# Optimization experiments

Hardware: AMD Instinct MI355X
Metric: run time of the kernel (lower is better)

Reference implementation:

```python
import jax, jax.numpy as jnp
import numpy as np

BITW = 1
BITA = 3
BATCH = 8192
IN_CH = 4096
N_UNITS = 4096


def _quantize(x, k):
    # DoReFa uniform quantizer with straight-through estimator (round -> identity grad)
    n = float(2 ** k - 1)
    return x + jax.lax.stop_gradient(jnp.round(x * n) / n - x)


def _cabs(x):
    # clip magnitude to [0, 1]
    return jnp.minimum(1.0, jnp.abs(x))


def quantize_active(x, bitA):
    if bitA == 32:
        return x
    return _quantize(x, bitA)


def quantize_weight(w, bitW):
    if bitW == 32:
        return w
    if bitW == 1:
        # binary weights scaled by mean |w| (E is treated as constant)
        E = jax.lax.stop_gradient(jnp.mean(jnp.abs(w)))
        y = w / E
        # sign with straight-through gradient
        return (y + jax.lax.stop_gradient(jnp.sign(y) - y)) * E
    t = jnp.tanh(w)
    t = t / jnp.max(jnp.abs(t)) * 0.5 + 0.5
    return 2.0 * _quantize(t, bitW) - 1.0


def setup_inputs() -> dict:
    key = jax.random.key(0)
    k1, k2 = jax.random.split(key)
    inputs = jax.random.normal(k1, (BATCH, IN_CH), dtype=jnp.float32)
    # truncated_normal(stddev=0.1) init approximated with normal * 0.1
    W = jax.random.normal(k2, (IN_CH, N_UNITS), dtype=jnp.float32) * 0.1
    b = jnp.zeros((N_UNITS,), dtype=jnp.float32)
    return {"inputs": inputs, "W": W, "b": b}


def reference(inputs, W, b):
    q_in = quantize_active(_cabs(inputs), BITA)   # [B, IN] in {0..1} grid of 2^bitA-1 levels
    q_W = quantize_weight(W, BITW)                # [IN, OUT] binary (+-E)
    out = jnp.matmul(q_in, q_W) + b               # [B, OUT]
    return out
```

## Files before the change

kernel.cpp:

```cpp
#include <hip/hip_runtime.h>


static constexpr int BATCH  = 8192;
static constexpr int IN_CH  = 4096;
static constexpr int NUNITS = 4096;
static constexpr int TPB    = 256;

typedef int v4i __attribute__((ext_vector_type(4)));

static constexpr size_t A8_OFF   = 0;
static constexpr size_t A8_BYTES = (size_t)BATCH * IN_CH;
static constexpr size_t BT_OFF   = A8_OFF + A8_BYTES;
static constexpr size_t BT_BYTES = (size_t)NUNITS * IN_CH;
static constexpr int    NPART    = 4096;
static constexpr size_t PART_OFF = BT_OFF + BT_BYTES;
static constexpr size_t SCALE_OFF= PART_OFF + NPART * sizeof(float);

__global__ __launch_bounds__(TPB) void k_scale(const float* __restrict__ partials,
                                               float* __restrict__ scale) {
    __shared__ float red[TPB];
    float s = 0.f;
    for (int i = threadIdx.x; i < NPART; i += TPB) s += partials[i];
    red[threadIdx.x] = s;
    __syncthreads();
    for (int off = TPB / 2; off > 0; off >>= 1) {
        if ((int)threadIdx.x < off) red[threadIdx.x] += red[threadIdx.x + off];
        __syncthreads();
    }
    if (threadIdx.x == 0) {
        float E = red[0] / (float)((size_t)IN_CH * NUNITS);
        *scale = E / 7.0f;
    }
}

__device__ __forceinline__ unsigned int q4(float4 v) {
    unsigned int b0 = (unsigned int)(int)rintf(fminf(1.0f, fabsf(v.x)) * 7.0f);
    unsigned int b1 = (unsigned int)(int)rintf(fminf(1.0f, fabsf(v.y)) * 7.0f);
    unsigned int b2 = (unsigned int)(int)rintf(fminf(1.0f, fabsf(v.z)) * 7.0f);
    unsigned int b3 = (unsigned int)(int)rintf(fminf(1.0f, fabsf(v.w)) * 7.0f);
    return b0 | (b1 << 8) | (b2 << 16) | (b3 << 24);
}

__global__ __launch_bounds__(TPB) void k_quant_a(const float4* __restrict__ x4,
                                                 uint4* __restrict__ a16) {
    const size_t t = (size_t)blockIdx.x * TPB + threadIdx.x;
    uint4 o;
    o.x = q4(x4[t * 4 + 0]);
    o.y = q4(x4[t * 4 + 1]);
    o.z = q4(x4[t * 4 + 2]);
    o.w = q4(x4[t * 4 + 3]);
    a16[t] = o;
}

__global__ __launch_bounds__(TPB) void k_signT(const float* __restrict__ W,
                                               char* __restrict__ bt,
                                               float* __restrict__ partials) {
    __shared__ char tile[64][68];
    __shared__ float red[TPB];
    const int bk = blockIdx.x & 63;
    const int bn = blockIdx.x >> 6;
    const int t  = threadIdx.x;
    const int c  = t & 63;
    const int r0 = t >> 6;
    float asum = 0.f;
#pragma unroll
    for (int i = 0; i < 16; ++i) {
        int r = i * 4 + r0;
        float w = W[(size_t)(bk * 64 + r) * NUNITS + bn * 64 + c];
        asum += fabsf(w);
        tile[c][r] = (w > 0.f) ? 1 : ((w < 0.f) ? -1 : 0);
    }
    __syncthreads();
    const int n  = t >> 2;
    const int kk = (t & 3) * 16;
    char o[16];
#pragma unroll
    for (int j = 0; j < 16; ++j) o[j] = tile[n][kk + j];
    *(uint4*)(bt + (size_t)(bn * 64 + n) * IN_CH + bk * 64 + kk) = *(const uint4*)o;

    red[t] = asum;
    __syncthreads();
    for (int off = TPB / 2; off > 0; off >>= 1) {
        if (t < off) red[t] += red[t + off];
        __syncthreads();
    }
    if (t == 0) partials[blockIdx.x] = red[0];
}

__device__ __forceinline__ void gload_lds16(const void* g, void* l) {
    __builtin_amdgcn_global_load_lds((const __attribute__((address_space(1))) void*)g,
                                     (__attribute__((address_space(3))) void*)l,
                                     16, 0, 0);
}

#define VMCNT8   asm volatile("s_waitcnt vmcnt(8)" ::: "memory")
#define VMCNT0   asm volatile("s_waitcnt vmcnt(0)" ::: "memory")
#define LGKM0    asm volatile("s_waitcnt lgkmcnt(0)" ::: "memory")
#define SCHEDB   __builtin_amdgcn_sched_barrier(0)
#define BARRIER  __builtin_amdgcn_s_barrier()

static constexpr int NT = IN_CH / 128;

__global__ __launch_bounds__(512, 2) void k_gemm(const char* __restrict__ A8,
                                                 const char* __restrict__ BT,
                                                 const float* __restrict__ scale_p,
                                                 const float* __restrict__ bias,
                                                 float* __restrict__ out) {
    __shared__ char As[2][32768];
    __shared__ char Bs[2][32768];

    const int t    = threadIdx.x;
    const int bid  = blockIdx.x;
    const int swzb = (bid & 7) * 64 + (bid >> 3);
    const int bRow = swzb >> 4;
    const int bCol = swzb & 15;
    const int lane = t & 63;
    const int wid  = t >> 6;
    const int wm   = wid >> 2;
    const int wn   = wid & 3;
    const int lr   = lane & 15;
    const int lk4  = lane >> 4;

    const size_t aBase = (size_t)(bRow * 256) * IN_CH;
    const size_t bBase = (size_t)(bCol * 256) * IN_CH;

    const int ceff0 = (lk4 * 16) ^ ((lr & 7) << 4);
    const int ceff1 = ceff0 ^ 64;

    const int srow  = t >> 3;
    const int scol  = ((t & 7) * 16) ^ ((srow & 7) << 4);
    const int sldso = t * 16;

    v4i acc[8][4] = {};

#define STAGE(kt, q)                                                                 \
    do {                                                                             \
        const int _b = (kt) & 1;                                                     \
        if ((q) < 4)                                                                 \
            gload_lds16(A8 + aBase + (size_t)((q) * 64 + srow) * IN_CH + (kt) * 128 + scol, \
                        &As[_b][(q & 3) * 8192 + sldso]);                            \
        else                                                                         \
            gload_lds16(BT + bBase + (size_t)(((q) - 4) * 64 + srow) * IN_CH + (kt) * 128 + scol, \
                        &Bs[_b][((q) - 4) * 8192 + sldso]);                          \
    } while (0)

#pragma unroll
    for (int q = 0; q < 8; ++q) STAGE(0, q);
#pragma unroll
    for (int q = 0; q < 8; ++q) STAGE(1, q);

    for (int kt = 0; kt < NT; ++kt) {
        const int buf = kt & 1;
        const char* Ab = As[buf];
        const char* Bb = Bs[buf];

        if (kt < NT - 1) { VMCNT8; } else { VMCNT0; }
        SCHEDB;
        BARRIER;
        v4i a0[4][2], a1[4][2], bf[4][2];
#pragma unroll
        for (int m = 0; m < 4; ++m) {
            const int ra0 = (wm * 128 + m * 16 + lr) * 128;
            const int ra1 = (wm * 128 + (m + 4) * 16 + lr) * 128;
            a0[m][0] = *(const v4i*)(Ab + ra0 + ceff0);
            a0[m][1] = *(const v4i*)(Ab + ra0 + ceff1);
            a1[m][0] = *(const v4i*)(Ab + ra1 + ceff0);
            a1[m][1] = *(const v4i*)(Ab + ra1 + ceff1);
        }
#pragma unroll
        for (int n = 0; n < 4; ++n) {
            const int rb = (wn * 64 + n * 16 + lr) * 128;
            bf[n][0] = *(const v4i*)(Bb + rb + ceff0);
            bf[n][1] = *(const v4i*)(Bb + rb + ceff1);
        }
        LGKM0;
        SCHEDB;
        BARRIER;
        __builtin_amdgcn_s_setprio(1);
#pragma unroll
        for (int m = 0; m < 4; ++m)
#pragma unroll
            for (int n = 0; n < 2; ++n)
#pragma unroll
                for (int s = 0; s < 2; ++s)
                    acc[m][n] = __builtin_amdgcn_mfma_i32_16x16x64_i8(a0[m][s], bf[n][s], acc[m][n], 0, 0, 0);
        __builtin_amdgcn_s_setprio(0);
        SCHEDB;

        if (kt + 2 < NT) { STAGE(kt + 2, 0); STAGE(kt + 2, 1); STAGE(kt + 2, 2); }
        SCHEDB;
        BARRIER;
        __builtin_amdgcn_s_setprio(1);
#pragma unroll
        for (int m = 0; m < 4; ++m)
#pragma unroll
            for (int n = 2; n < 4; ++n)
#pragma unroll
                for (int s = 0; s < 2; ++s)
                    acc[m][n] = __builtin_amdgcn_mfma_i32_16x16x64_i8(a0[m][s], bf[n][s], acc[m][n], 0, 0, 0);
        __builtin_amdgcn_s_setprio(0);
        SCHEDB;

        if (kt + 2 < NT) { STAGE(kt + 2, 3); STAGE(kt + 2, 4); STAGE(kt + 2, 5); }
        SCHEDB;
        BARRIER;
        __builtin_amdgcn_s_setprio(1);
#pragma unroll
        for (int m = 0; m < 4; ++m)
#pragma unroll
            for (int n = 0; n < 2; ++n)
#pragma unroll
                for (int s = 0; s < 2; ++s)
                    acc[m + 4][n] = __builtin_amdgcn_mfma_i32_16x16x64_i8(a1[m][s], bf[n][s], acc[m + 4][n], 0, 0, 0);
        __builtin_amdgcn_s_setprio(0);
        SCHEDB;

        if (kt + 2 < NT) { STAGE(kt + 2, 6); STAGE(kt + 2, 7); }
        SCHEDB;
        BARRIER;
        __builtin_amdgcn_s_setprio(1);
#pragma unroll
        for (int m = 0; m < 4; ++m)
#pragma unroll
            for (int n = 2; n < 4; ++n)
#pragma unroll
                for (int s = 0; s < 2; ++s)
                    acc[m + 4][n] = __builtin_amdgcn_mfma_i32_16x16x64_i8(a1[m][s], bf[n][s], acc[m + 4][n], 0, 0, 0);
        __builtin_amdgcn_s_setprio(0);
        SCHEDB;
    }

    const float scale = *scale_p;
    const int orow0 = bRow * 256 + wm * 128;
    const int ocol0 = bCol * 256 + wn * 64;
#pragma unroll
    for (int m = 0; m < 8; ++m) {
#pragma unroll
        for (int n = 0; n < 4; ++n) {
            const int col = ocol0 + n * 16 + lr;
            const float bb = bias[col];
            const int rbase = orow0 + m * 16 + lk4 * 4;
#pragma unroll
            for (int j = 0; j < 4; ++j)
                out[(size_t)(rbase + j) * NUNITS + col] = scale * (float)acc[m][n][j] + bb;
        }
    }
#undef STAGE
}

extern "C" void kernel_launch(void* const* d_in, const int* in_sizes, int n_in,
                              void* d_out, int out_size, void* d_ws, size_t ws_size,
                              hipStream_t stream) {
    const float* x  = (const float*)d_in[0];
    const float* W  = (const float*)d_in[1];
    const float* b  = (const float*)d_in[2];
    float* out      = (float*)d_out;

    char*  ws       = (char*)d_ws;
    char*  A8       = ws + A8_OFF;
    char*  BT       = ws + BT_OFF;
    float* partials = (float*)(ws + PART_OFF);
    float* scale    = (float*)(ws + SCALE_OFF);

    k_signT<<<(IN_CH / 64) * (NUNITS / 64), TPB, 0, stream>>>(W, BT, partials);
    k_scale<<<1, TPB, 0, stream>>>(partials, scale);
    k_quant_a<<<(BATCH * (IN_CH / 16)) / TPB, TPB, 0, stream>>>((const float4*)x, (uint4*)A8);
    k_gemm<<<(BATCH / 256) * (NUNITS / 256), 512, 0, stream>>>(A8, BT, scale, b, out);
}
```

Before: 185.0 us.

## Interleave LDS fragment reads with MFMA quarters in unrolled two-tile GEMM loop

Restructures the int8 GEMM main loop into a 2x-unrolled, 8-phase schedule. Each phase reads only the A/B LDS fragments it needs, issues a couple of global->LDS stage loads for the next tile, and runs 16 MFMAs. This replaces the single bulk LDS read per k-tile. The goal is to overlap LDS reads and global prefetch with MFMA work and shrink the register-fragment footprint, at the cost of more barriers per tile and a tighter buffer-reuse schedule that relies on careful vmcnt ordering.

```diff
diff --git a/kernel.cpp b/kernel.cpp
--- a/kernel.cpp
+++ b/kernel.cpp
@@ -93,11 +93,13 @@
                                      16, 0, 0);
 }
 
-#define VMCNT8   asm volatile("s_waitcnt vmcnt(8)" ::: "memory")
+#define VMCNT2   asm volatile("s_waitcnt vmcnt(2)" ::: "memory")
 #define VMCNT0   asm volatile("s_waitcnt vmcnt(0)" ::: "memory")
 #define LGKM0    asm volatile("s_waitcnt lgkmcnt(0)" ::: "memory")
 #define SCHEDB   __builtin_amdgcn_sched_barrier(0)
 #define BARRIER  __builtin_amdgcn_s_barrier()
+#define PRIO1    __builtin_amdgcn_s_setprio(1)
+#define PRIO0    __builtin_amdgcn_s_setprio(0)
 
 static constexpr int NT = IN_CH / 128;
 
@@ -132,102 +134,101 @@
     const int sldso = t * 16;
 
     v4i acc[8][4] = {};
-
-#define STAGE(kt, q)                                                                 \
-    do {                                                                             \
-        const int _b = (kt) & 1;                                                     \
-        if ((q) < 4)                                                                 \
+    v4i a0[4][2], a1[4][2], b01[2][2], b23[2][2];
+
+#define STAGE(kt, q)                                                                  \
+    do {                                                                              \
+        const int _b = (kt) & 1;                                                      \
+        if ((q) < 4)                                                                  \
             gload_lds16(A8 + aBase + (size_t)((q) * 64 + srow) * IN_CH + (kt) * 128 + scol, \
-                        &As[_b][(q & 3) * 8192 + sldso]);                            \
-        else                                                                         \
+                        &As[_b][(q & 3) * 8192 + sldso]);                             \
+        else                                                                          \
             gload_lds16(BT + bBase + (size_t)(((q) - 4) * 64 + srow) * IN_CH + (kt) * 128 + scol, \
-                        &Bs[_b][((q) - 4) * 8192 + sldso]);                          \
+                        &Bs[_b][((q) - 4) * 8192 + sldso]);                           \
     } while (0)
 
+#define READ_A0(Ab)                                                    \
+    _Pragma("unroll") for (int m = 0; m < 4; ++m) {                    \
+        const int ra = (wm * 128 + m * 16 + lr) * 128;                 \
+        a0[m][0] = *(const v4i*)((Ab) + ra + ceff0);                   \
+        a0[m][1] = *(const v4i*)((Ab) + ra + ceff1);                   \
+    }
+#define READ_A1(Ab)                                                    \
+    _Pragma("unroll") for (int m = 0; m < 4; ++m) {                    \
+        const int ra = (wm * 128 + (m + 4) * 16 + lr) * 128;           \
+        a1[m][0] = *(const v4i*)((Ab) + ra + ceff0);                   \
+        a1[m][1] = *(const v4i*)((Ab) + ra + ceff1);                   \
+    }
+#define READ_B01(Bb)                                                   \
+    _Pragma("unroll") for (int n = 0; n < 2; ++n) {                    \
+        const int rb = (wn * 64 + n * 16 + lr) * 128;                  \
+        b01[n][0] = *(const v4i*)((Bb) + rb + ceff0);                  \
+        b01[n][1] = *(const v4i*)((Bb) + rb + ceff1);                  \
+    }
+#define READ_B23(Bb)                                                   \
+    _Pragma("unroll") for (int n = 0; n < 2; ++n) {                    \
+        const int rb = (wn * 64 + (n + 2) * 16 + lr) * 128;            \
+        b23[n][0] = *(const v4i*)((Bb) + rb + ceff0);                  \
+        b23[n][1] = *(const v4i*)((Bb) + rb + ceff1);                  \
+    }
+#define MFMA16(arr, brr, mo, no)                                                       \
+    PRIO1;                                                                             \
+    _Pragma("unroll") for (int m = 0; m < 4; ++m)                                      \
+        _Pragma("unroll") for (int n = 0; n < 2; ++n)                                  \
+            _Pragma("unroll") for (int s = 0; s < 2; ++s)                              \
+                acc[(mo) + m][(no) + n] = __builtin_amdgcn_mfma_i32_16x16x64_i8(       \
+                    arr[m][s], brr[n][s], acc[(mo) + m][(no) + n], 0, 0, 0);           \
+    PRIO0
+
 #pragma unroll
     for (int q = 0; q < 8; ++q) STAGE(0, q);
-#pragma unroll
-    for (int q = 0; q < 8; ++q) STAGE(1, q);
-
-    for (int kt = 0; kt < NT; ++kt) {
-        const int buf = kt & 1;
-        const char* Ab = As[buf];
-        const char* Bb = Bs[buf];
-
-        if (kt < NT - 1) { VMCNT8; } else { VMCNT0; }
-        SCHEDB;
-        BARRIER;
-        v4i a0[4][2], a1[4][2], bf[4][2];
-#pragma unroll
-        for (int m = 0; m < 4; ++m) {
-            const int ra0 = (wm * 128 + m * 16 + lr) * 128;
-            const int ra1 = (wm * 128 + (m + 4) * 16 + lr) * 128;
-            a0[m][0] = *(const v4i*)(Ab + ra0 + ceff0);
-            a0[m][1] = *(const v4i*)(Ab + ra0 + ceff1);
-            a1[m][0] = *(const v4i*)(Ab + ra1 + ceff0);
-            a1[m][1] = *(const v4i*)(Ab + ra1 + ceff1);
-        }
-#pragma unroll
-        for (int n = 0; n < 4; ++n) {
-            const int rb = (wn * 64 + n * 16 + lr) * 128;
-            bf[n][0] = *(const v4i*)(Bb + rb + ceff0);
-            bf[n][1] = *(const v4i*)(Bb + rb + ceff1);
-        }
-        LGKM0;
-        SCHEDB;
-        BARRIER;
-        __builtin_amdgcn_s_setprio(1);
-#pragma unroll
-        for (int m = 0; m < 4; ++m)
-#pragma unroll
-            for (int n = 0; n < 2; ++n)
-#pragma unroll
-                for (int s = 0; s < 2; ++s)
-                    acc[m][n] = __builtin_amdgcn_mfma_i32_16x16x64_i8(a0[m][s], bf[n][s], acc[m][n], 0, 0, 0);
-        __builtin_amdgcn_s_setprio(0);
-        SCHEDB;
-
-        if (kt + 2 < NT) { STAGE(kt + 2, 0); STAGE(kt + 2, 1); STAGE(kt + 2, 2); }
-        SCHEDB;
-        BARRIER;
-        __builtin_amdgcn_s_setprio(1);
-#pragma unroll
-        for (int m = 0; m < 4; ++m)
-#pragma unroll
-            for (int n = 2; n < 4; ++n)
-#pragma unroll
-                for (int s = 0; s < 2; ++s)
-                    acc[m][n] = __builtin_amdgcn_mfma_i32_16x16x64_i8(a0[m][s], bf[n][s], acc[m][n], 0, 0, 0);
-        __builtin_amdgcn_s_setprio(0);
-        SCHEDB;
-
-        if (kt + 2 < NT) { STAGE(kt + 2, 3); STAGE(kt + 2, 4); STAGE(kt + 2, 5); }
-        SCHEDB;
-        BARRIER;
-        __builtin_amdgcn_s_setprio(1);
-#pragma unroll
-        for (int m = 0; m < 4; ++m)
-#pragma unroll
-            for (int n = 0; n < 2; ++n)
-#pragma unroll
-                for (int s = 0; s < 2; ++s)
-                    acc[m + 4][n] = __builtin_amdgcn_mfma_i32_16x16x64_i8(a1[m][s], bf[n][s], acc[m + 4][n], 0, 0, 0);
-        __builtin_amdgcn_s_setprio(0);
-        SCHEDB;
-
-        if (kt + 2 < NT) { STAGE(kt + 2, 6); STAGE(kt + 2, 7); }
-        SCHEDB;
-        BARRIER;
-        __builtin_amdgcn_s_setprio(1);
-#pragma unroll
-        for (int m = 0; m < 4; ++m)
-#pragma unroll
-            for (int n = 2; n < 4; ++n)
-#pragma unroll
-                for (int s = 0; s < 2; ++s)
-                    acc[m + 4][n] = __builtin_amdgcn_mfma_i32_16x16x64_i8(a1[m][s], bf[n][s], acc[m + 4][n], 0, 0, 0);
-        __builtin_amdgcn_s_setprio(0);
-        SCHEDB;
+    STAGE(1, 0); STAGE(1, 1);
+    VMCNT2; SCHEDB;
+    BARRIER;
+
+    for (int T = 0; T < NT; T += 2) {
+        const char* Ab0 = As[0]; const char* Bb0 = Bs[0];
+        const char* Ab1 = As[1]; const char* Bb1 = Bs[1];
+        const bool more = (T + 2 < NT);
+
+        READ_A0(Ab0); READ_B01(Bb0);
+        STAGE(T + 1, 2); STAGE(T + 1, 3);
+        SCHEDB; BARRIER; LGKM0; SCHEDB;
+        MFMA16(a0, b01, 0, 0); SCHEDB; BARRIER;
+
+        READ_B23(Bb0);
+        STAGE(T + 1, 4); STAGE(T + 1, 5);
+        SCHEDB; BARRIER; LGKM0; SCHEDB;
+        MFMA16(a0, b23, 0, 2); SCHEDB; BARRIER;
+
+        READ_A1(Ab0);
+        STAGE(T + 1, 6); STAGE(T + 1, 7);
+        SCHEDB; BARRIER; LGKM0; SCHEDB;
+        MFMA16(a1, b01, 4, 0); SCHEDB; BARRIER;
+
+        if (more) { STAGE(T + 2, 0); STAGE(T + 2, 1); VMCNT2; }
+        else      { VMCNT0; }
+        SCHEDB; BARRIER; SCHEDB;
+        MFMA16(a1, b23, 4, 2); SCHEDB; BARRIER;
+
+        READ_A0(Ab1); READ_B01(Bb1);
+        if (more) { STAGE(T + 2, 2); STAGE(T + 2, 3); }
+        SCHEDB; BARRIER; LGKM0; SCHEDB;
+        MFMA16(a0, b01, 0, 0); SCHEDB; BARRIER;
+
+        READ_B23(Bb1);
+        if (more) { STAGE(T + 2, 4); STAGE(T + 2, 5); }
+        SCHEDB; BARRIER; LGKM0; SCHEDB;
+        MFMA16(a0, b23, 0, 2); SCHEDB; BARRIER;
+
+        READ_A1(Ab1);
+        if (more) { STAGE(T + 2, 6); STAGE(T + 2, 7); }
+        SCHEDB; BARRIER; LGKM0; SCHEDB;
+        MFMA16(a1, b01, 4, 0); SCHEDB; BARRIER;
+
+        if (more) { STAGE(T + 3, 0); STAGE(T + 3, 1); VMCNT2; }
+        SCHEDB; BARRIER; SCHEDB;
+        MFMA16(a1, b23, 4, 2); SCHEDB; BARRIER;
     }
 
     const float scale = *scale_p;
@@ -246,6 +247,11 @@
         }
     }
 #undef STAGE
+#undef READ_A0
+#undef READ_A1
+#undef READ_B01
+#undef READ_B23
+#undef MFMA16
 }
 
 extern "C" void kernel_launch(void* const* d_in, const int* in_sizes, int n_in,
```

New measurement: 195.1 us. +5.5%, slower.
